# Optimization experiments

Hardware: AMD Instinct MI355X
Metric: run time of the kernel (lower is better)

## Reference

```python
import jax, jax.numpy as jnp
import numpy as np
from jax import lax

B, SEQ, C, H, W, OUT, K = 64, 32, 16, 128, 256, 10, 2  # batch, timestamps, channels, hidden, width, classes, substeps/interval


def setup_inputs() -> dict:
    key = jax.random.key(0)
    ks = jax.random.split(key, 16)
    p = lambda k, shape, fan_in: (jax.random.normal(k, shape, dtype=jnp.float32) / np.sqrt(fan_in))
    coeff = lambda k: jax.random.normal(k, (B, SEQ - 1, C), dtype=jnp.float32)
    return {
        'ts': jnp.arange(SEQ, dtype=jnp.float32),
        'coeff_d': coeff(ks[0]), 'coeff_c': coeff(ks[1]), 'coeff_b': coeff(ks[2]), 'coeff_a': coeff(ks[3]),
        # initial MLP: in_size -> width -> width -> hidden (relu)
        'iw0': p(ks[4], (W, C), C), 'ib0': jnp.zeros((W,), jnp.float32),
        'iw1': p(ks[5], (W, W), W), 'ib1': jnp.zeros((W,), jnp.float32),
        'iw2': p(ks[6], (H, W), W), 'ib2': jnp.zeros((H,), jnp.float32),
        # vector-field MLP: hidden -> width -> width -> hidden*in_size (softplus, tanh final)
        'fw0': p(ks[7], (W, H), H), 'fb0': jnp.zeros((W,), jnp.float32),
        'fw1': p(ks[8], (W, W), W), 'fb1': jnp.zeros((W,), jnp.float32),
        'fw2': p(ks[9], (H * C, W), W), 'fb2': jnp.zeros((H * C,), jnp.float32),
        # readout linear: hidden -> out
        'lw': p(ks[10], (OUT, H), H), 'lb': jnp.zeros((OUT,), jnp.float32),
    }


def _forward(ts, coeff_d, coeff_c, coeff_b, coeff_a, iw0, ib0, iw1, ib1, iw2, ib2,
             fw0, fb0, fw1, fb1, fw2, fb2, lw, lb):
    nb, ni, c = coeff_a.shape
    h_dim = iw2.shape[0]

    def init_mlp(x):  # [B,C] -> [B,H]
        h = jax.nn.relu(x @ iw0.T + ib0)
        h = jax.nn.relu(h @ iw1.T + ib1)
        return h @ iw2.T + ib2

    def vf(y):  # [B,H] -> [B,H,C]
        h = jax.nn.softplus(y @ fw0.T + fb0)
        h = jax.nn.softplus(h @ fw1.T + fb1)
        return jnp.tanh(h @ fw2.T + fb2).reshape(nb, h_dim, c)

    def dxdt(frac, i):  # derivative of cubic interpolation on interval i: 3d f^2 + 2c f + b
        return (3.0 * coeff_d[:, i] * frac + 2.0 * coeff_c[:, i]) * frac + coeff_b[:, i]

    def f(frac, i, y):  # ControlTerm.to_ode: dy/dt = vf(y) @ dX/dt
        return jnp.einsum('bhc,bc->bh', vf(y), dxdt(frac, i))

    dts = jnp.diff(ts)
    hsub = dts / K
    idx = jnp.repeat(jnp.arange(ni), K)                                # interval index per substep
    hs = jnp.repeat(hsub, K)                                           # substep size
    fr0 = jnp.tile(jnp.arange(K, dtype=ts.dtype), ni) * hs             # offset within interval at substep start

    def step(y, xs):  # one fixed-size Tsit5 step (Tsitouras 2011 tableau)
        t0, h, i = xs
        k1 = f(t0, i, y)
        k2 = f(t0 + 0.161 * h, i, y + h * (0.161 * k1))
        k3 = f(t0 + 0.327 * h, i, y + h * (-0.008480655492356989 * k1 + 0.335480655492357 * k2))
        k4 = f(t0 + 0.9 * h, i, y + h * (2.8971530571054935 * k1 - 6.359448489975075 * k2 + 4.3622954328695815 * k3))
        k5 = f(t0 + 0.9800255409045097 * h, i, y + h * (5.325864828439257 * k1 - 11.748883564062828 * k2 + 7.4955393428898365 * k3 - 0.09249506636175525 * k4))
        k6 = f(t0 + h, i, y + h * (5.86145544294642 * k1 - 12.92096931784711 * k2 + 8.159367898576159 * k3 - 0.071584973281401 * k4 - 0.028269050394068383 * k5))
        y_new = y + h * (0.09646076681806523 * k1 + 0.01 * k2 + 0.4798896504144996 * k3 + 1.379008574103742 * k4 - 3.290069515436081 * k5 + 2.324710524099774 * k6)
        return y_new, None

    y0 = init_mlp(coeff_a[:, 0])  # X(ts[0]) = a-coefficient at frac=0
    yT, _ = lax.scan(step, y0, (fr0, hs, idx))
    return jax.nn.log_softmax(yT @ lw.T + lb, axis=-1)  # out_size != 1 -> log_softmax


def reference(ts, coeff_d, coeff_c, coeff_b, coeff_a, iw0, ib0, iw1, ib1, iw2, ib2,
              fw0, fb0, fw1, fb1, fw2, fb2, lw, lb):
    return _forward(ts, coeff_d, coeff_c, coeff_b, coeff_a, iw0, ib0, iw1, ib1, iw2, ib2,
                    fw0, fb0, fw1, fb1, fw2, fb2, lw, lb)
```

## Files before the change

### kernel.cpp

```cpp
#include <hip/hip_runtime.h>

#define NBATCH 64
#define NSEQ   32
#define NI     31
#define NC     16
#define NH     128
#define NW     256
#define NOUT   10
#define NSUB   62

#define NGRP 8
#define GB   8
#define NSL  32
#define NBLK (NGRP*NSL)
#define BS   512

#define L1R 8
#define L2R 8
#define L3H 4
#define L3R 64

#define P128 132
#define P256 260

#define WS_BAR   0
#define WS_H1    16384
#define WS_H2    (16384 + 65536)
#define WS_KV    (16384 + 131072)

__device__ const float ATAB[6][5] = {
  {0.f, 0.f, 0.f, 0.f, 0.f},
  {0.161f, 0.f, 0.f, 0.f, 0.f},
  {-0.008480655492356989f, 0.335480655492357f, 0.f, 0.f, 0.f},
  {2.8971530571054935f, -6.359448489975075f, 4.3622954328695815f, 0.f, 0.f},
  {5.325864828439257f, -11.748883564062828f, 7.4955393428898365f, -0.09249506636175525f, 0.f},
  {5.86145544294642f, -12.92096931784711f, 8.159367898576159f, -0.071584973281401f, -0.028269050394068383f}
};
__device__ const float CNODE[6] = {0.f, 0.161f, 0.327f, 0.9f, 0.9800255409045097f, 1.f};
__device__ const float BTAB[6]  = {0.09646076681806523f, 0.01f, 0.4798896504144996f,
                                   1.379008574103742f, -3.290069515436081f, 2.324710524099774f};

__device__ __forceinline__ float softplusf_(float x) {
  return fmaxf(x, 0.0f) + log1pf(expf(-fabsf(x)));
}
__device__ __forceinline__ float dot4(float4 a, float4 b) {
  return (a.x*b.x + a.y*b.y) + (a.z*b.z + a.w*b.w);
}

__device__ __forceinline__ void gstore(float* p, float v) {
  __hip_atomic_store(p, v, __ATOMIC_RELAXED, __HIP_MEMORY_SCOPE_AGENT);
}
__device__ __forceinline__ float gload(const float* p) {
  return __hip_atomic_load(p, __ATOMIC_RELAXED, __HIP_MEMORY_SCOPE_AGENT);
}

#define SLOT_STRIDE 16
__device__ __forceinline__ void group_barrier(unsigned* slots, int myslot, unsigned seq) {
  __syncthreads();
  if (threadIdx.x == 0) {
    __hip_atomic_store(&slots[myslot * SLOT_STRIDE], seq,
                       __ATOMIC_RELAXED, __HIP_MEMORY_SCOPE_AGENT);
  }
  if (threadIdx.x < 64) {
    const int lane = threadIdx.x & 31;
    for (;;) {
      const unsigned v = __hip_atomic_load(&slots[lane * SLOT_STRIDE],
                                           __ATOMIC_RELAXED, __HIP_MEMORY_SCOPE_AGENT);
      if (__all(v >= seq)) break;
      __builtin_amdgcn_s_sleep(2);
    }
  }
  __syncthreads();
}

__global__ void bar_init(unsigned* bar) {
  const int n = NGRP * NSL * SLOT_STRIDE;
  for (int i = threadIdx.x; i < n; i += blockDim.x)
    __hip_atomic_store(&bar[i], 0u, __ATOMIC_RELAXED, __HIP_MEMORY_SCOPE_AGENT);
}

__global__ __launch_bounds__(BS) void ncde_fwd(
    const float* __restrict__ ts,
    const float* __restrict__ cd, const float* __restrict__ cc,
    const float* __restrict__ cb, const float* __restrict__ ca,
    const float* __restrict__ iw0, const float* __restrict__ ib0,
    const float* __restrict__ iw1, const float* __restrict__ ib1,
    const float* __restrict__ iw2, const float* __restrict__ ib2,
    const float* __restrict__ fw0, const float* __restrict__ fb0,
    const float* __restrict__ fw1, const float* __restrict__ fb1,
    const float* __restrict__ fw2, const float* __restrict__ fb2,
    const float* __restrict__ lw,  const float* __restrict__ lb,
    unsigned* __restrict__ bar, float* __restrict__ h1g, float* __restrict__ h2g,
    float* __restrict__ kvg, float* __restrict__ out)
{
  const int t   = threadIdx.x;
  const int g   = blockIdx.x & 7;
  const int s   = blockIdx.x >> 3;
  const int gr0 = g * GB;
  unsigned* slots = bar + g * NSL * SLOT_STRIDE;
  unsigned  bseq  = 0;

  __shared__ float fw0s[L1R][P128];
  __shared__ float fw1s[L2R][P256];
  __shared__ float fw2s[L3R][P256];
  __shared__ float h1s[GB][P256];
  __shared__ float h2s[GB][P256];
  __shared__ float ysv[GB][P128];
  __shared__ float yloc[GB][NH];
  __shared__ float dxs[GB][NC];
  __shared__ float x0s[GB][NC];
  __shared__ float fb0s[L1R], fb1s[L2R], fb2s[L3R];
  __shared__ float tss[NSEQ];
  __shared__ float lgs[GB][NOUT], lses[GB];

  {
    if (t < 256) {
      int row = t >> 5, j = t & 31;
      *(float4*)&fw0s[row][4*j] = *(const float4*)&fw0[(size_t)(s*L1R + row)*NH + 4*j];
    }
    {
      int r2 = t >> 6, j2 = t & 63;
      *(float4*)&fw1s[r2][4*j2] = *(const float4*)&fw1[(size_t)(s*L2R + r2)*NW + 4*j2];
    }
    #pragma unroll
    for (int i = 0; i < 8; ++i) {
      int e = t + BS*i; int r2 = e >> 6, j2 = e & 63;
      *(float4*)&fw2s[r2][4*j2] = *(const float4*)&fw2[(size_t)(s*L3R + r2)*NW + 4*j2];
    }
    if (t < L1R) fb0s[t] = fb0[s*L1R + t];
    if (t < L2R) fb1s[t] = fb1[s*L2R + t];
    if (t < L3R) fb2s[t] = fb2[s*L3R + t];
    if (t < NSEQ) tss[t] = ts[t];
  }

  if (t < GB*NC) { int r = t >> 4, c = t & 15; x0s[r][c] = ca[((size_t)(gr0 + r)*NI)*NC + c]; }
  __syncthreads();
  #pragma unroll
  for (int i = 0; i < 4; ++i) {
    int e = t + BS*i; int r = e >> 8, row = e & 255;
    float a = ib0[row];
    #pragma unroll
    for (int k = 0; k < NC; ++k) a += iw0[row*NC + k] * x0s[r][k];
    h1s[r][row] = fmaxf(a, 0.f);
  }
  __syncthreads();
  #pragma unroll
  for (int i = 0; i < 4; ++i) {
    int e = t + BS*i; int r = e >> 8, row = e & 255;
    float a = ib1[row];
    const float4* wr = (const float4*)&iw1[(size_t)row*NW];
    for (int k = 0; k < 64; ++k) a += dot4(wr[k], *(const float4*)&h1s[r][4*k]);
    h2s[r][row] = fmaxf(a, 0.f);
  }
  __syncthreads();
  #pragma unroll
  for (int i = 0; i < 2; ++i) {
    int e = t + BS*i; int r = e >> 7, row = e & 127;
    float a = ib2[row];
    const float4* wr = (const float4*)&iw2[(size_t)row*NW];
    for (int k = 0; k < 64; ++k) a += dot4(wr[k], *(const float4*)&h2s[r][4*k]);
    yloc[r][row] = a;
  }
  __syncthreads();

  const int yr  = t >> 5, yc4 = 4*(t & 31);
  const int o   = t >> 3, q8 = t & 7;
  const int orow = o & 7, obat = o >> 3;
  const int l3row = t & 63, l3h = l3row >> 4, l3c = l3row & 15, l3b = t >> 6;

  float4 yreg, kreg[6];
  if (t < 256) yreg = *(const float4*)&yloc[yr][yc4];

  for (int ss = 0; ss < NSUB; ++ss) {
    const int iv = ss >> 1, jv = ss & 1;
    const float h = (tss[iv+1] - tss[iv]) * 0.5f;
    const float t0f = (float)jv * h;

    float cdv = 0.f, ccv = 0.f, cbv = 0.f;
    if (t >= 256 && t < 256 + GB*NC) {
      const int tc = t - 256;
      const size_t base = ((size_t)(gr0 + (tc >> 4))*NI + iv)*NC + (tc & 15);
      cdv = cd[base]; ccv = cc[base]; cbv = cb[base];
    }

    for (int st = 0; st < 6; ++st) {
      if (t < 256) {
        float4 v = yreg;
        for (int jj = 0; jj < st; ++jj) {
          const float a = h * ATAB[st][jj];
          v.x += a*kreg[jj].x; v.y += a*kreg[jj].y;
          v.z += a*kreg[jj].z; v.w += a*kreg[jj].w;
        }
        *(float4*)&ysv[yr][yc4] = v;
      } else if (t < 256 + GB*NC) {
        const int tc = t - 256;
        const float f = t0f + CNODE[st] * h;
        dxs[tc >> 4][tc & 15] = (3.f*cdv*f + 2.f*ccv)*f + cbv;
      }
      __syncthreads();

      {
        float a0 = 0.f, a1 = 0.f;
        #pragma unroll
        for (int i = 0; i < 4; i += 2) {
          a0 += dot4(*(const float4*)&fw0s[orow][4*(q8+8*i)],     *(const float4*)&ysv[obat][4*(q8+8*i)]);
          a1 += dot4(*(const float4*)&fw0s[orow][4*(q8+8*(i+1))], *(const float4*)&ysv[obat][4*(q8+8*(i+1))]);
        }
        float a = a0 + a1;
        a += __shfl_xor(a, 1); a += __shfl_xor(a, 2); a += __shfl_xor(a, 4);
        if (q8 == 0) gstore(&h1g[(gr0 + obat)*NW + s*L1R + orow], softplusf_(fb0s[orow] + a));
      }
      group_barrier(slots, s, ++bseq);

      #pragma unroll
      for (int i = 0; i < 4; ++i) {
        int e = t + BS*i; int r = e >> 8, col = e & 255;
        h1s[r][col] = gload(&h1g[(gr0 + r)*NW + col]);
      }
      __syncthreads();

      {
        float a0 = 0.f, a1 = 0.f;
        #pragma unroll
        for (int i = 0; i < 8; i += 2) {
          a0 += dot4(*(const float4*)&fw1s[orow][4*(q8+8*i)],     *(const float4*)&h1s[obat][4*(q8+8*i)]);
          a1 += dot4(*(const float4*)&fw1s[orow][4*(q8+8*(i+1))], *(const float4*)&h1s[obat][4*(q8+8*(i+1))]);
        }
        float a = a0 + a1;
        a += __shfl_xor(a, 1); a += __shfl_xor(a, 2); a += __shfl_xor(a, 4);
        if (q8 == 0) gstore(&h2g[(gr0 + obat)*NW + s*L2R + orow], softplusf_(fb1s[orow] + a));
      }
      group_barrier(slots, s, ++bseq);

      #pragma unroll
      for (int i = 0; i < 4; ++i) {
        int e = t + BS*i; int r = e >> 8, col = e & 255;
        h2s[r][col] = gload(&h2g[(gr0 + r)*NW + col]);
      }
      __syncthreads();

      {
        const float4* wr = (const float4*)&fw2s[l3row][0];
        const float4* xr = (const float4*)&h2s[l3b][0];
        float a0 = 0.f, a1 = 0.f, a2 = 0.f, a3 = 0.f;
        #pragma unroll 4
        for (int i = 0; i < 64; i += 4) {
          a0 += dot4(wr[i+0], xr[i+0]);
          a1 += dot4(wr[i+1], xr[i+1]);
          a2 += dot4(wr[i+2], xr[i+2]);
          a3 += dot4(wr[i+3], xr[i+3]);
        }
        float v0 = tanhf(((a0+a1)+(a2+a3)) + fb2s[l3row]) * dxs[l3b][l3c];
        v0 += __shfl_xor(v0, 1);
        v0 += __shfl_xor(v0, 2);
        v0 += __shfl_xor(v0, 4);
        v0 += __shfl_xor(v0, 8);
        if (l3c == 0) gstore(&kvg[((size_t)st*NBATCH + gr0 + l3b)*NH + s*L3H + l3h], v0);
      }
      group_barrier(slots, s, ++bseq);

      if (t < 256) {
        const float* kp = &kvg[((size_t)st*NBATCH + gr0 + yr)*NH + yc4];
        kreg[st].x = gload(kp+0); kreg[st].y = gload(kp+1);
        kreg[st].z = gload(kp+2); kreg[st].w = gload(kp+3);
      }
    }

    if (t < 256) {
      #pragma unroll
      for (int s2 = 0; s2 < 6; ++s2) {
        const float a = h * BTAB[s2];
        yreg.x += a*kreg[s2].x; yreg.y += a*kreg[s2].y;
        yreg.z += a*kreg[s2].z; yreg.w += a*kreg[s2].w;
      }
    }
  }

  if (t < 256) *(float4*)&yloc[yr][yc4] = yreg;
  __syncthreads();

  if (s == 0) {
    if (t < GB*NOUT) {
      const int r = t / NOUT, oo = t % NOUT;
      float a = lb[oo];
      const float4* wr = (const float4*)&lw[(size_t)oo*NH];
      #pragma unroll
      for (int k = 0; k < 32; ++k) a += dot4(wr[k], *(const float4*)&yloc[r][4*k]);
      lgs[r][oo] = a;
    }
    __syncthreads();
    if (t < GB) {
      float m = lgs[t][0];
      for (int oo = 1; oo < NOUT; ++oo) m = fmaxf(m, lgs[t][oo]);
      float se = 0.f;
      for (int oo = 0; oo < NOUT; ++oo) se += expf(lgs[t][oo] - m);
      lses[t] = m + logf(se);
    }
    __syncthreads();
    if (t < GB*NOUT) {
      const int r = t / NOUT, oo = t % NOUT;
      out[(gr0 + r)*NOUT + oo] = lgs[r][oo] - lses[r];
    }
  }
}

extern "C" void kernel_launch(void* const* d_in, const int* in_sizes, int n_in,
                              void* d_out, int out_size, void* d_ws, size_t ws_size,
                              hipStream_t stream) {
  const float* ts  = (const float*)d_in[0];
  const float* cd  = (const float*)d_in[1];
  const float* cc  = (const float*)d_in[2];
  const float* cb  = (const float*)d_in[3];
  const float* ca  = (const float*)d_in[4];
  const float* iw0 = (const float*)d_in[5];
  const float* ib0 = (const float*)d_in[6];
  const float* iw1 = (const float*)d_in[7];
  const float* ib1 = (const float*)d_in[8];
  const float* iw2 = (const float*)d_in[9];
  const float* ib2 = (const float*)d_in[10];
  const float* fw0 = (const float*)d_in[11];
  const float* fb0 = (const float*)d_in[12];
  const float* fw1 = (const float*)d_in[13];
  const float* fb1 = (const float*)d_in[14];
  const float* fw2 = (const float*)d_in[15];
  const float* fb2 = (const float*)d_in[16];
  const float* lw  = (const float*)d_in[17];
  const float* lb  = (const float*)d_in[18];

  char* ws = (char*)d_ws;
  unsigned* bar = (unsigned*)(ws + WS_BAR);
  float* h1g = (float*)(ws + WS_H1);
  float* h2g = (float*)(ws + WS_H2);
  float* kvg = (float*)(ws + WS_KV);

  bar_init<<<1, 512, 0, stream>>>(bar);
  ncde_fwd<<<NBLK, BS, 0, stream>>>(ts, cd, cc, cb, ca, iw0, ib0, iw1, ib1, iw2, ib2,
                                    fw0, fb0, fw1, fb1, fw2, fb2, lw, lb,
                                    bar, h1g, h2g, kvg, (float*)d_out);
}
```

Measured before the change: 4.136 ms.

## Replace group barriers with tagged 64-bit value+phase dataflow synchronization

Removes the slot-based group barrier between layers. Each exchanged activation is now stored as a 64-bit word holding the float and a phase tag, and readers spin until every word they need carries the expected tag. This merges barrier and data load into one round trip and removes an extra __syncthreads plus the flag polling. The cost is twice the bytes per exchanged value, more polling traffic on global memory, and a larger tag-init kernel.

```diff
diff --git a/kernel.cpp b/kernel.cpp
--- a/kernel.cpp
+++ b/kernel.cpp
@@ -23,10 +23,10 @@
 #define P128 132
 #define P256 260
 
-#define WS_BAR   0
-#define WS_H1    16384
-#define WS_H2    (16384 + 65536)
-#define WS_KV    (16384 + 131072)
+#define WS_H1    0
+#define WS_H2    (128*1024)
+#define WS_KV    (256*1024)
+#define WS_TOTAL_U64 (2*64*256 + 6*64*128)
 
 __device__ const float ATAB[6][5] = {
   {0.f, 0.f, 0.f, 0.f, 0.f},
@@ -47,36 +47,24 @@
   return (a.x*b.x + a.y*b.y) + (a.z*b.z + a.w*b.w);
 }
 
-__device__ __forceinline__ void gstore(float* p, float v) {
+typedef unsigned long long u64;
+__device__ __forceinline__ u64 gload64(const u64* p) {
+  return __hip_atomic_load(p, __ATOMIC_RELAXED, __HIP_MEMORY_SCOPE_AGENT);
+}
+__device__ __forceinline__ void gstore64(u64* p, u64 v) {
   __hip_atomic_store(p, v, __ATOMIC_RELAXED, __HIP_MEMORY_SCOPE_AGENT);
 }
-__device__ __forceinline__ float gload(const float* p) {
-  return __hip_atomic_load(p, __ATOMIC_RELAXED, __HIP_MEMORY_SCOPE_AGENT);
-}
-
-#define SLOT_STRIDE 16
-__device__ __forceinline__ void group_barrier(unsigned* slots, int myslot, unsigned seq) {
-  __syncthreads();
-  if (threadIdx.x == 0) {
-    __hip_atomic_store(&slots[myslot * SLOT_STRIDE], seq,
-                       __ATOMIC_RELAXED, __HIP_MEMORY_SCOPE_AGENT);
-  }
-  if (threadIdx.x < 64) {
-    const int lane = threadIdx.x & 31;
-    for (;;) {
-      const unsigned v = __hip_atomic_load(&slots[lane * SLOT_STRIDE],
-                                           __ATOMIC_RELAXED, __HIP_MEMORY_SCOPE_AGENT);
-      if (__all(v >= seq)) break;
-      __builtin_amdgcn_s_sleep(2);
-    }
-  }
-  __syncthreads();
-}
-
-__global__ void bar_init(unsigned* bar) {
-  const int n = NGRP * NSL * SLOT_STRIDE;
-  for (int i = threadIdx.x; i < n; i += blockDim.x)
-    __hip_atomic_store(&bar[i], 0u, __ATOMIC_RELAXED, __HIP_MEMORY_SCOPE_AGENT);
+__device__ __forceinline__ u64 packvt(float v, unsigned tag) {
+  return ((u64)tag << 32) | (u64)__float_as_uint(v);
+}
+
+__global__ void tag_init(u64* ws) {
+  const int idx = blockIdx.x * blockDim.x + threadIdx.x;
+  #pragma unroll
+  for (int i = 0; i < 5; ++i) {
+    const int e = idx + 16384*i;
+    if (e < WS_TOTAL_U64) gstore64(&ws[e], 0ull);
+  }
 }
 
 __global__ __launch_bounds__(BS) void ncde_fwd(
@@ -90,15 +78,13 @@
     const float* __restrict__ fw1, const float* __restrict__ fb1,
     const float* __restrict__ fw2, const float* __restrict__ fb2,
     const float* __restrict__ lw,  const float* __restrict__ lb,
-    unsigned* __restrict__ bar, float* __restrict__ h1g, float* __restrict__ h2g,
-    float* __restrict__ kvg, float* __restrict__ out)
+    u64* __restrict__ h1g, u64* __restrict__ h2g,
+    u64* __restrict__ kvg, float* __restrict__ out)
 {
   const int t   = threadIdx.x;
   const int g   = blockIdx.x & 7;
   const int s   = blockIdx.x >> 3;
   const int gr0 = g * GB;
-  unsigned* slots = bar + g * NSL * SLOT_STRIDE;
-  unsigned  bseq  = 0;
 
   __shared__ float fw0s[L1R][P128];
   __shared__ float fw1s[L2R][P256];
@@ -171,6 +157,8 @@
   float4 yreg, kreg[6];
   if (t < 256) yreg = *(const float4*)&yloc[yr][yc4];
 
+  unsigned p = 0;
+
   for (int ss = 0; ss < NSUB; ++ss) {
     const int iv = ss >> 1, jv = ss & 1;
     const float h = (tss[iv+1] - tss[iv]) * 0.5f;
@@ -184,6 +172,9 @@
     }
 
     for (int st = 0; st < 6; ++st) {
+      const unsigned ph1 = p + 1, ph2 = p + 2, phk = p + 3;
+      p += 3;
+
       if (t < 256) {
         float4 v = yreg;
         for (int jj = 0; jj < st; ++jj) {
@@ -208,14 +199,28 @@
         }
         float a = a0 + a1;
         a += __shfl_xor(a, 1); a += __shfl_xor(a, 2); a += __shfl_xor(a, 4);
-        if (q8 == 0) gstore(&h1g[(gr0 + obat)*NW + s*L1R + orow], softplusf_(fb0s[orow] + a));
-      }
-      group_barrier(slots, s, ++bseq);
-
-      #pragma unroll
-      for (int i = 0; i < 4; ++i) {
-        int e = t + BS*i; int r = e >> 8, col = e & 255;
-        h1s[r][col] = gload(&h1g[(gr0 + r)*NW + col]);
+        if (q8 == 0)
+          gstore64(&h1g[(gr0 + obat)*NW + s*L1R + orow], packvt(softplusf_(fb0s[orow] + a), ph1));
+      }
+
+      {
+        const u64* basep = h1g + (size_t)gr0 * NW;
+        u64 vv[4];
+        for (;;) {
+          bool ok = true;
+          #pragma unroll
+          for (int i = 0; i < 4; ++i) {
+            vv[i] = gload64(basep + t + BS*i);
+            ok &= ((unsigned)(vv[i] >> 32) == ph1);
+          }
+          if (ok) break;
+          __builtin_amdgcn_s_sleep(1);
+        }
+        #pragma unroll
+        for (int i = 0; i < 4; ++i) {
+          const int e = t + BS*i;
+          h1s[e >> 8][e & 255] = __uint_as_float((unsigned)vv[i]);
+        }
       }
       __syncthreads();
 
@@ -228,14 +233,28 @@
         }
         float a = a0 + a1;
         a += __shfl_xor(a, 1); a += __shfl_xor(a, 2); a += __shfl_xor(a, 4);
-        if (q8 == 0) gstore(&h2g[(gr0 + obat)*NW + s*L2R + orow], softplusf_(fb1s[orow] + a));
-      }
-      group_barrier(slots, s, ++bseq);
-
-      #pragma unroll
-      for (int i = 0; i < 4; ++i) {
-        int e = t + BS*i; int r = e >> 8, col = e & 255;
-        h2s[r][col] = gload(&h2g[(gr0 + r)*NW + col]);
+        if (q8 == 0)
+          gstore64(&h2g[(gr0 + obat)*NW + s*L2R + orow], packvt(softplusf_(fb1s[orow] + a), ph2));
+      }
+
+      {
+        const u64* basep = h2g + (size_t)gr0 * NW;
+        u64 vv[4];
+        for (;;) {
+          bool ok = true;
+          #pragma unroll
+          for (int i = 0; i < 4; ++i) {
+            vv[i] = gload64(basep + t + BS*i);
+            ok &= ((unsigned)(vv[i] >> 32) == ph2);
+          }
+          if (ok) break;
+          __builtin_amdgcn_s_sleep(1);
+        }
+        #pragma unroll
+        for (int i = 0; i < 4; ++i) {
+          const int e = t + BS*i;
+          h2s[e >> 8][e & 255] = __uint_as_float((unsigned)vv[i]);
+        }
       }
       __syncthreads();
 
@@ -255,14 +274,27 @@
         v0 += __shfl_xor(v0, 2);
         v0 += __shfl_xor(v0, 4);
         v0 += __shfl_xor(v0, 8);
-        if (l3c == 0) gstore(&kvg[((size_t)st*NBATCH + gr0 + l3b)*NH + s*L3H + l3h], v0);
-      }
-      group_barrier(slots, s, ++bseq);
+        if (l3c == 0)
+          gstore64(&kvg[((size_t)st*NBATCH + gr0 + l3b)*NH + s*L3H + l3h], packvt(v0, phk));
+      }
 
       if (t < 256) {
-        const float* kp = &kvg[((size_t)st*NBATCH + gr0 + yr)*NH + yc4];
-        kreg[st].x = gload(kp+0); kreg[st].y = gload(kp+1);
-        kreg[st].z = gload(kp+2); kreg[st].w = gload(kp+3);
+        const u64* kp = &kvg[((size_t)st*NBATCH + gr0 + yr)*NH + yc4];
+        u64 vv[4];
+        for (;;) {
+          bool ok = true;
+          #pragma unroll
+          for (int i = 0; i < 4; ++i) {
+            vv[i] = gload64(kp + i);
+            ok &= ((unsigned)(vv[i] >> 32) == phk);
+          }
+          if (ok) break;
+          __builtin_amdgcn_s_sleep(1);
+        }
+        kreg[st].x = __uint_as_float((unsigned)vv[0]);
+        kreg[st].y = __uint_as_float((unsigned)vv[1]);
+        kreg[st].z = __uint_as_float((unsigned)vv[2]);
+        kreg[st].w = __uint_as_float((unsigned)vv[3]);
       }
     }
 
@@ -328,13 +360,12 @@
   const float* lb  = (const float*)d_in[18];
 
   char* ws = (char*)d_ws;
-  unsigned* bar = (unsigned*)(ws + WS_BAR);
-  float* h1g = (float*)(ws + WS_H1);
-  float* h2g = (float*)(ws + WS_H2);
-  float* kvg = (float*)(ws + WS_KV);
-
-  bar_init<<<1, 512, 0, stream>>>(bar);
+  u64* h1g = (u64*)(ws + WS_H1);
+  u64* h2g = (u64*)(ws + WS_H2);
+  u64* kvg = (u64*)(ws + WS_KV);
+
+  tag_init<<<64, 256, 0, stream>>>((u64*)ws);
   ncde_fwd<<<NBLK, BS, 0, stream>>>(ts, cd, cc, cb, ca, iw0, ib0, iw1, ib1, iw2, ib2,
                                     fw0, fb0, fw1, fb1, fw2, fb2, lw, lb,
-                                    bar, h1g, h2g, kvg, (float*)d_out);
-}
+                                    h1g, h2g, kvg, (float*)d_out);
+}
```

Result: slower. 5.454 ms (+31.9%).

## Pack inter-block exchange buffers contiguously and use vector coherent loads/stores

Applied to the files above, without the earlier changes.

Reorganises the global scratch buffers used to exchange per-slice MLP activations and RK stage vectors between the 32 blocks of a group, so that each group's data is contiguous and each thread fetches one float4. Exchange now uses dwordx4 loads and stores with sc0 sc1 cache bypass via inline asm, replacing many scalar atomic loads. Stage-3 results are packed into one vector store per wave. The change also adds an explicit vmcnt wait before the barrier and shortens the spin sleep. The aim is to cut the latency and instruction count of the cross-block communication in each of the many barrier phases, at the cost of hand-written memory ordering that must stay correct.

```diff
diff --git a/kernel.cpp b/kernel.cpp
--- a/kernel.cpp
+++ b/kernel.cpp
@@ -27,6 +27,8 @@
 #define WS_H1    16384
 #define WS_H2    (16384 + 65536)
 #define WS_KV    (16384 + 131072)
+
+typedef float f4v __attribute__((ext_vector_type(4)));
 
 __device__ const float ATAB[6][5] = {
   {0.f, 0.f, 0.f, 0.f, 0.f},
@@ -47,15 +49,22 @@
   return (a.x*b.x + a.y*b.y) + (a.z*b.z + a.w*b.w);
 }
 
-__device__ __forceinline__ void gstore(float* p, float v) {
+__device__ __forceinline__ void sta_f32(float* p, float v) {
   __hip_atomic_store(p, v, __ATOMIC_RELAXED, __HIP_MEMORY_SCOPE_AGENT);
 }
-__device__ __forceinline__ float gload(const float* p) {
-  return __hip_atomic_load(p, __ATOMIC_RELAXED, __HIP_MEMORY_SCOPE_AGENT);
+__device__ __forceinline__ void sta_f32x4(float* p, f4v v) {
+  asm volatile("global_store_dwordx4 %0, %1, off sc0 sc1" :: "v"(p), "v"(v) : "memory");
+}
+__device__ __forceinline__ f4v lda_f32x4(const float* p) {
+  f4v r;
+  asm volatile("global_load_dwordx4 %0, %1, off sc0 sc1\n\ts_waitcnt vmcnt(0)"
+               : "=v"(r) : "v"(p) : "memory");
+  return r;
 }
 
 #define SLOT_STRIDE 16
 __device__ __forceinline__ void group_barrier(unsigned* slots, int myslot, unsigned seq) {
+  asm volatile("s_waitcnt vmcnt(0)" ::: "memory");
   __syncthreads();
   if (threadIdx.x == 0) {
     __hip_atomic_store(&slots[myslot * SLOT_STRIDE], seq,
@@ -67,7 +76,7 @@
       const unsigned v = __hip_atomic_load(&slots[lane * SLOT_STRIDE],
                                            __ATOMIC_RELAXED, __HIP_MEMORY_SCOPE_AGENT);
       if (__all(v >= seq)) break;
-      __builtin_amdgcn_s_sleep(2);
+      __builtin_amdgcn_s_sleep(1);
     }
   }
   __syncthreads();
@@ -90,8 +99,8 @@
     const float* __restrict__ fw1, const float* __restrict__ fb1,
     const float* __restrict__ fw2, const float* __restrict__ fb2,
     const float* __restrict__ lw,  const float* __restrict__ lb,
-    unsigned* __restrict__ bar, float* __restrict__ h1g, float* __restrict__ h2g,
-    float* __restrict__ kvg, float* __restrict__ out)
+    unsigned* __restrict__ bar, float* __restrict__ h1c, float* __restrict__ h2c,
+    float* __restrict__ kvc, float* __restrict__ out)
 {
   const int t   = threadIdx.x;
   const int g   = blockIdx.x & 7;
@@ -99,6 +108,9 @@
   const int gr0 = g * GB;
   unsigned* slots = bar + g * NSL * SLOT_STRIDE;
   unsigned  bseq  = 0;
+  float* h1cg = h1c + g * (NSL*GB*L1R);
+  float* h2cg = h2c + g * (NSL*GB*L2R);
+  float* kvcg = kvc + g * (6*NSL*GB*4);
 
   __shared__ float fw0s[L1R][P128];
   __shared__ float fw1s[L2R][P256];
@@ -163,12 +175,14 @@
   }
   __syncthreads();
 
-  const int yr  = t >> 5, yc4 = 4*(t & 31);
-  const int o   = t >> 3, q8 = t & 7;
+  const int lane = t & 63;
+  const int w    = t >> 6;
+  const int yr   = t >> 5, yc4 = 4*(t & 31);
+  const int o    = t >> 3, q8 = t & 7;
   const int orow = o & 7, obat = o >> 3;
-  const int l3row = t & 63, l3h = l3row >> 4, l3c = l3row & 15, l3b = t >> 6;
-
-  float4 yreg, kreg[6];
+  const int l3row = t & 63, l3c = t & 15, l3b = t >> 6;
+
+  float4 yreg; f4v kreg[6];
   if (t < 256) yreg = *(const float4*)&yloc[yr][yc4];
 
   for (int ss = 0; ss < NSUB; ++ss) {
@@ -188,8 +202,8 @@
         float4 v = yreg;
         for (int jj = 0; jj < st; ++jj) {
           const float a = h * ATAB[st][jj];
-          v.x += a*kreg[jj].x; v.y += a*kreg[jj].y;
-          v.z += a*kreg[jj].z; v.w += a*kreg[jj].w;
+          v.x += a*kreg[jj][0]; v.y += a*kreg[jj][1];
+          v.z += a*kreg[jj][2]; v.w += a*kreg[jj][3];
         }
         *(float4*)&ysv[yr][yc4] = v;
       } else if (t < 256 + GB*NC) {
@@ -208,14 +222,15 @@
         }
         float a = a0 + a1;
         a += __shfl_xor(a, 1); a += __shfl_xor(a, 2); a += __shfl_xor(a, 4);
-        if (q8 == 0) gstore(&h1g[(gr0 + obat)*NW + s*L1R + orow], softplusf_(fb0s[orow] + a));
+        const float praw = __shfl(a, (lane & 7) * 8);
+        if (lane < 8)
+          sta_f32(&h1cg[(s*GB + w)*L1R + lane], softplusf_(fb0s[lane] + praw));
       }
       group_barrier(slots, s, ++bseq);
 
-      #pragma unroll
-      for (int i = 0; i < 4; ++i) {
-        int e = t + BS*i; int r = e >> 8, col = e & 255;
-        h1s[r][col] = gload(&h1g[(gr0 + r)*NW + col]);
+      {
+        const f4v v = lda_f32x4(h1cg + 4*t);
+        *(f4v*)&h1s[(t >> 1) & 7][(t >> 4)*8 + 4*(t & 1)] = v;
       }
       __syncthreads();
 
@@ -228,14 +243,15 @@
         }
         float a = a0 + a1;
         a += __shfl_xor(a, 1); a += __shfl_xor(a, 2); a += __shfl_xor(a, 4);
-        if (q8 == 0) gstore(&h2g[(gr0 + obat)*NW + s*L2R + orow], softplusf_(fb1s[orow] + a));
+        const float praw = __shfl(a, (lane & 7) * 8);
+        if (lane < 8)
+          sta_f32(&h2cg[(s*GB + w)*L2R + lane], softplusf_(fb1s[lane] + praw));
       }
       group_barrier(slots, s, ++bseq);
 
-      #pragma unroll
-      for (int i = 0; i < 4; ++i) {
-        int e = t + BS*i; int r = e >> 8, col = e & 255;
-        h2s[r][col] = gload(&h2g[(gr0 + r)*NW + col]);
+      {
+        const f4v v = lda_f32x4(h2cg + 4*t);
+        *(f4v*)&h2s[(t >> 1) & 7][(t >> 4)*8 + 4*(t & 1)] = v;
       }
       __syncthreads();
 
@@ -255,14 +271,16 @@
         v0 += __shfl_xor(v0, 2);
         v0 += __shfl_xor(v0, 4);
         v0 += __shfl_xor(v0, 8);
-        if (l3c == 0) gstore(&kvg[((size_t)st*NBATCH + gr0 + l3b)*NH + s*L3H + l3h], v0);
+        f4v pk;
+        pk[0] = __shfl(v0, 0);  pk[1] = __shfl(v0, 16);
+        pk[2] = __shfl(v0, 32); pk[3] = __shfl(v0, 48);
+        if (lane == 0)
+          sta_f32x4(&kvcg[((st*NSL + s)*GB + w)*4], pk);
       }
       group_barrier(slots, s, ++bseq);
 
       if (t < 256) {
-        const float* kp = &kvg[((size_t)st*NBATCH + gr0 + yr)*NH + yc4];
-        kreg[st].x = gload(kp+0); kreg[st].y = gload(kp+1);
-        kreg[st].z = gload(kp+2); kreg[st].w = gload(kp+3);
+        kreg[st] = lda_f32x4(kvcg + ((st*NSL + (t & 31))*GB + yr)*4);
       }
     }
 
@@ -270,8 +288,8 @@
       #pragma unroll
       for (int s2 = 0; s2 < 6; ++s2) {
         const float a = h * BTAB[s2];
-        yreg.x += a*kreg[s2].x; yreg.y += a*kreg[s2].y;
-        yreg.z += a*kreg[s2].z; yreg.w += a*kreg[s2].w;
+        yreg.x += a*kreg[s2][0]; yreg.y += a*kreg[s2][1];
+        yreg.z += a*kreg[s2][2]; yreg.w += a*kreg[s2][3];
       }
     }
   }
@@ -329,12 +347,12 @@
 
   char* ws = (char*)d_ws;
   unsigned* bar = (unsigned*)(ws + WS_BAR);
-  float* h1g = (float*)(ws + WS_H1);
-  float* h2g = (float*)(ws + WS_H2);
-  float* kvg = (float*)(ws + WS_KV);
+  float* h1c = (float*)(ws + WS_H1);
+  float* h2c = (float*)(ws + WS_H2);
+  float* kvc = (float*)(ws + WS_KV);
 
   bar_init<<<1, 512, 0, stream>>>(bar);
   ncde_fwd<<<NBLK, BS, 0, stream>>>(ts, cd, cc, cb, ca, iw0, ib0, iw1, ib1, iw2, ib2,
                                     fw0, fb0, fw1, fb1, fw2, fb2, lw, lb,
-                                    bar, h1g, h2g, kvg, (float*)d_out);
-}
+                                    bar, h1c, h2c, kvc, (float*)d_out);
+}
```

Measured after the change: 4.266 ms. +3.1%, slower.
